# Performance work log

Measured on AMD Instinct MI355X. Metric: run time of the kernel, lower is better.

Reference implementation:

```python
import jax, jax.numpy as jnp
import numpy as np

B, T, H, DEPTH = 16, 2048, 256, 3

def setup_inputs() -> dict:
    key = jax.random.key(0)
    ks = jax.random.split(key, 5)
    x = jax.random.normal(ks[0], (B, T, H), dtype=jnp.float32)
    seq_lens = jax.random.randint(ks[1], (B,), 1, T + 1, dtype=jnp.int32)
    s = 1.0 / np.sqrt(H)
    W_ih = jax.random.uniform(ks[2], (DEPTH, H, H), jnp.float32, -s, s)
    W_hh = jax.random.uniform(ks[3], (DEPTH, H, H), jnp.float32, -s, s)
    b = jax.random.uniform(ks[4], (DEPTH, H), jnp.float32, -s, s)
    return {"x": x, "seq_lens": seq_lens, "W_ih": W_ih, "W_hh": W_hh, "b": b}

def reference(x, seq_lens, W_ih, W_hh, b):
    # x: [B, T, D], stacked depth-3 single-state recurrent cells:
    #   h[t,k] = tanh(inp @ W_ih[k]^T + h[t-1,k] @ W_hh[k]^T + b[k])
    # where inp = x[t] for k==0 else h[t,k-1]; h[-1,k] = 0 (init_state).
    Bx, Tx, D = x.shape
    depth = W_ih.shape[0]
    h0 = jnp.zeros((depth, Bx, D), dtype=x.dtype)

    def step(h_prev, x_t):  # h_prev: [depth, B, H], x_t: [B, D]
        inp = x_t
        hs = []
        for k in range(depth):
            hk = jnp.tanh(inp @ W_ih[k].T + h_prev[k] @ W_hh[k].T + b[k])
            hs.append(hk)
            inp = hk
        h_new = jnp.stack(hs)  # [depth, B, H]
        return h_new, h_new

    _, ys = jax.lax.scan(step, h0, jnp.swapaxes(x, 0, 1))  # ys: [T, depth, B, H]
    out = jnp.transpose(ys, (2, 0, 1, 3))  # [B, T, depth, H]
    # positions past each sequence's length are never written (stay zero)
    mask = (jnp.arange(Tx)[None, :] < seq_lens[:, None])[:, :, None, None]
    return out * mask.astype(out.dtype)
```

## Files before the change

kernel.cpp:

```cpp
#include <hip/hip_runtime.h>
#include <stdint.h>


#define TT 2048
#define HH 256

typedef _Float16 h16x8 __attribute__((ext_vector_type(8)));
typedef float f32x4 __attribute__((ext_vector_type(4)));

__device__ __forceinline__ unsigned pkrtz(float a, float b) {
  return __builtin_bit_cast(unsigned, __builtin_amdgcn_cvt_pkrtz(a, b));
}

__device__ __forceinline__ float tanh_fast(float x) {
  float xm = fmaxf(x, -15.0f);
  float e = __builtin_amdgcn_exp2f(xm * -2.88539008177793f);
  float r = __builtin_amdgcn_rcpf(1.0f + e);
  return __builtin_fmaf(-2.0f * e, r, 1.0f);
}

__device__ __forceinline__ void spin_ge(int* p, int need) {
  while (__hip_atomic_load(p, __ATOMIC_ACQUIRE, __HIP_MEMORY_SCOPE_AGENT) < need)
    __builtin_amdgcn_s_sleep(2);
}

__device__ __forceinline__ void light_barrier() {
  asm volatile("s_waitcnt expcnt(0) lgkmcnt(0)" ::: "memory");
  __builtin_amdgcn_s_barrier();
}

__global__ __launch_bounds__(512, 2)
void stacked_rnn(const float* __restrict__ x,
                 const int* __restrict__ seq_lens,
                 const float* __restrict__ Wih,
                 const float* __restrict__ Whh,
                 const float* __restrict__ bias,
                 float* __restrict__ out,
                 int* flags) {
  const int ks = blockIdx.x;
  const int tid = (int)threadIdx.x;
  const int w = tid >> 6;
  const int lane = tid & 63;
  const int q = lane >> 4;
  const int n = lane & 15;

  __shared__ __align__(16) unsigned short Bsm[2][8192];

  int* flag_up = flags + (ks - 1) * 64;
  int* flag_me = flags + ks * 64;

  h16x8 wf[2][16];
  {
    const float* wih_s = Wih + ks * (HH * HH);
    const float* whh_s = Whh + ks * (HH * HH);
#pragma unroll
    for (int mti = 0; mti < 2; ++mti) {
      const int fA = w * 32 + mti * 16 + n;
#pragma unroll
      for (int kt = 0; kt < 16; ++kt) {
        const int col = (kt & 7) * 32 + q * 8;
        const float* src = (kt < 8) ? (wih_s + fA * HH + col)
                                    : (whh_s + fA * HH + col);
        float4 a0 = ((const float4*)src)[0];
        float4 a1 = ((const float4*)src)[1];
        h16x8 f;
        f[0] = (_Float16)a0.x; f[1] = (_Float16)a0.y;
        f[2] = (_Float16)a0.z; f[3] = (_Float16)a0.w;
        f[4] = (_Float16)a1.x; f[5] = (_Float16)a1.y;
        f[6] = (_Float16)a1.z; f[7] = (_Float16)a1.w;
        wf[mti][kt] = f;
      }
    }
  }

  f32x4 biasv[2];
#pragma unroll
  for (int mti = 0; mti < 2; ++mti)
#pragma unroll
    for (int r = 0; r < 4; ++r)
      biasv[mti][r] = bias[ks * HH + w * 32 + mti * 16 + q * 4 + r];

  const int sl = seq_lens[n];

  const int rdE = (q * 16 + (n ^ q)) * 8;
  const int rdO = (q * 16 + (n ^ q ^ 4)) * 8;

  int hofs[2];
#pragma unroll
  for (int mti = 0; mti < 2; ++mti) {
    const int u = (8 + w) * 4 + mti * 2 + (q >> 1);
    hofs[mti] = (u * 16 + (n ^ (u & 7))) * 8 + (q & 1) * 4;
  }

  const int n_l = tid >> 5;
  const int k8  = tid & 31;
  const int u_l = (k8 >> 2) * 4 + (k8 & 3);
  const int ldst = (u_l * 16 + (n_l ^ (u_l & 7))) * 8;

  const float* src_base;
  int src_stride;
  if (ks == 0) {
    src_base = x + ((n_l * TT) << 8) + (k8 << 3);
    src_stride = HH;
  } else {
    src_base = out + (((n_l * TT) * 3 + (ks - 1)) << 8) + (k8 << 3);
    src_stride = 3 * HH;
  }

  ((uint4*)&Bsm[0][4096])[tid] = make_uint4(0, 0, 0, 0);
  if (ks > 0 && tid == 0) spin_ge(flag_up, 18);
  __syncthreads();

  {
    float4 c0 = ((const float4*)src_base)[0];
    float4 c1 = ((const float4*)src_base)[1];
    *(uint4*)&Bsm[0][ldst] = make_uint4(pkrtz(c0.x, c0.y), pkrtz(c0.z, c0.w),
                                        pkrtz(c1.x, c1.y), pkrtz(c1.z, c1.w));
  }
  float4 pfB0 = ((const float4*)(src_base + src_stride))[0];
  float4 pfB1 = ((const float4*)(src_base + src_stride))[1];
  const float* src_pf = src_base + 2 * src_stride;
  __syncthreads();

  float* outp = out + ((n * TT) * 3 + ks) * HH + w * 32 + q * 4;

  for (int t = 0; t < TT; ++t) {
    unsigned short* Bp = Bsm[t & 1];
    unsigned short* Bq = Bsm[(t & 1) ^ 1];

    if ((t & 7) == 0 && t > 0 && ks < 2 && tid == 0)
      __hip_atomic_store(flag_me, t, __ATOMIC_RELEASE,
                         __HIP_MEMORY_SCOPE_AGENT);
    if ((t & 15) == 0 && t > 0 && ks > 0) {
      if (tid == 0) {
        int need = t + 18;
        if (need > TT) need = TT;
        spin_ge(flag_up, need);
      }
      __syncthreads();
    }

    float4 pfA0, pfA1;
    const bool more2 = (t + 2 < TT);
    if (more2) {
      pfA0 = ((const float4*)src_pf)[0];
      pfA1 = ((const float4*)src_pf)[1];
    }
    src_pf += src_stride;

    f32x4 acc[2] = {biasv[0], biasv[1]};
#pragma unroll
    for (int kt = 0; kt < 16; ++kt) {
      const int ofs = ((kt & 1) ? rdO : rdE) + kt * 512;
      h16x8 bf = *(const h16x8*)&Bp[ofs];
      acc[0] = __builtin_amdgcn_mfma_f32_16x16x32_f16(wf[0][kt], bf, acc[0], 0, 0, 0);
      acc[1] = __builtin_amdgcn_mfma_f32_16x16x32_f16(wf[1][kt], bf, acc[1], 0, 0, 0);
    }

    const bool live = (t < sl);
    uint2 hpk[2];
#pragma unroll
    for (int mti = 0; mti < 2; ++mti) {
      float h0 = tanh_fast(acc[mti][0]);
      float h1 = tanh_fast(acc[mti][1]);
      float h2 = tanh_fast(acc[mti][2]);
      float h3 = tanh_fast(acc[mti][3]);
      hpk[mti].x = pkrtz(h0, h1);
      hpk[mti].y = pkrtz(h2, h3);
      float4 od;
      od.x = live ? h0 : 0.0f;
      od.y = live ? h1 : 0.0f;
      od.z = live ? h2 : 0.0f;
      od.w = live ? h3 : 0.0f;
      *(float4*)(outp + mti * 16) = od;
    }
    outp += 3 * HH;

    if (t + 1 < TT) {
      *(uint4*)&Bq[ldst] = make_uint4(pkrtz(pfB0.x, pfB0.y), pkrtz(pfB0.z, pfB0.w),
                                      pkrtz(pfB1.x, pfB1.y), pkrtz(pfB1.z, pfB1.w));
      *(uint2*)&Bq[hofs[0]] = hpk[0];
      *(uint2*)&Bq[hofs[1]] = hpk[1];
      if (more2) { pfB0 = pfA0; pfB1 = pfA1; }
    }

    if ((t & 7) == 7) {
      __syncthreads();
    } else {
      light_barrier();
    }
  }

  if (ks < 2 && tid == 0)
    __hip_atomic_store(flag_me, TT, __ATOMIC_RELEASE, __HIP_MEMORY_SCOPE_AGENT);
}

extern "C" void kernel_launch(void* const* d_in, const int* in_sizes, int n_in,
                              void* d_out, int out_size, void* d_ws, size_t ws_size,
                              hipStream_t stream) {
  (void)in_sizes; (void)n_in; (void)out_size; (void)ws_size;
  const float* x   = (const float*)d_in[0];
  const int*   sl  = (const int*)d_in[1];
  const float* wih = (const float*)d_in[2];
  const float* whh = (const float*)d_in[3];
  const float* b   = (const float*)d_in[4];

  (void)hipMemsetAsync(d_ws, 0, 1024, stream);
  hipLaunchKernelGGL(stacked_rnn, dim3(3), dim3(512), 0, stream,
                     x, sl, wih, whh, b, (float*)d_out, (int*)d_ws);
}
```

Measured before the change: 2.242 ms.

## Split waves into input-projection producers and recurrent-math consumers with LDS handoff

New measurement: 7.356 ms. +228.2%, slower.

```diff
diff --git a/kernel.cpp b/kernel.cpp
--- a/kernel.cpp
+++ b/kernel.cpp
@@ -10,6 +10,12 @@
 
 __device__ __forceinline__ unsigned pkrtz(float a, float b) {
   return __builtin_bit_cast(unsigned, __builtin_amdgcn_cvt_pkrtz(a, b));
+}
+
+__device__ __forceinline__ h16x8 pack8(float4 a, float4 b) {
+  uint4 u = make_uint4(pkrtz(a.x, a.y), pkrtz(a.z, a.w),
+                       pkrtz(b.x, b.y), pkrtz(b.z, b.w));
+  return __builtin_bit_cast(h16x8, u);
 }
 
 __device__ __forceinline__ float tanh_fast(float x) {
@@ -39,28 +45,28 @@
                  int* flags) {
   const int ks = blockIdx.x;
   const int tid = (int)threadIdx.x;
-  const int w = tid >> 6;
+  const int w8 = tid >> 6;
+  const bool is_math = (w8 < 4);
+  const int mw = w8 & 3;
   const int lane = tid & 63;
   const int q = lane >> 4;
   const int n = lane & 15;
 
-  __shared__ __align__(16) unsigned short Bsm[2][8192];
+  __shared__ __align__(16) unsigned short Hsm[2][4096];
+  __shared__ __align__(16) float Psm[2][4096];
 
   int* flag_up = flags + (ks - 1) * 64;
   int* flag_me = flags + ks * 64;
 
-  h16x8 wf[2][16];
+  h16x8 wf[4][8];
   {
-    const float* wih_s = Wih + ks * (HH * HH);
-    const float* whh_s = Whh + ks * (HH * HH);
-#pragma unroll
-    for (int mti = 0; mti < 2; ++mti) {
-      const int fA = w * 32 + mti * 16 + n;
-#pragma unroll
-      for (int kt = 0; kt < 16; ++kt) {
-        const int col = (kt & 7) * 32 + q * 8;
-        const float* src = (kt < 8) ? (wih_s + fA * HH + col)
-                                    : (whh_s + fA * HH + col);
+    const float* wsrc = (is_math ? Whh : Wih) + ks * (HH * HH);
+#pragma unroll
+    for (int mti = 0; mti < 4; ++mti) {
+      const int fA = mw * 64 + mti * 16 + n;
+#pragma unroll
+      for (int kt = 0; kt < 8; ++kt) {
+        const float* src = wsrc + fA * HH + kt * 32 + q * 8;
         float4 a0 = ((const float4*)src)[0];
         float4 a1 = ((const float4*)src)[1];
         h16x8 f;
@@ -73,61 +79,61 @@
     }
   }
 
-  f32x4 biasv[2];
-#pragma unroll
-  for (int mti = 0; mti < 2; ++mti)
+  f32x4 biasv[4];
+#pragma unroll
+  for (int mti = 0; mti < 4; ++mti)
 #pragma unroll
     for (int r = 0; r < 4; ++r)
-      biasv[mti][r] = bias[ks * HH + w * 32 + mti * 16 + q * 4 + r];
+      biasv[mti][r] = bias[ks * HH + mw * 64 + mti * 16 + q * 4 + r];
 
   const int sl = seq_lens[n];
 
   const int rdE = (q * 16 + (n ^ q)) * 8;
   const int rdO = (q * 16 + (n ^ q ^ 4)) * 8;
-
-  int hofs[2];
-#pragma unroll
-  for (int mti = 0; mti < 2; ++mti) {
-    const int u = (8 + w) * 4 + mti * 2 + (q >> 1);
+  int hofs[4];
+#pragma unroll
+  for (int mti = 0; mti < 4; ++mti) {
+    const int u = mw * 8 + mti * 2 + (q >> 1);
     hofs[mti] = (u * 16 + (n ^ (u & 7))) * 8 + (q & 1) * 4;
   }
-
-  const int n_l = tid >> 5;
-  const int k8  = tid & 31;
-  const int u_l = (k8 >> 2) * 4 + (k8 & 3);
-  const int ldst = (u_l * 16 + (n_l ^ (u_l & 7))) * 8;
-
-  const float* src_base;
-  int src_stride;
-  if (ks == 0) {
-    src_base = x + ((n_l * TT) << 8) + (k8 << 3);
-    src_stride = HH;
-  } else {
-    src_base = out + (((n_l * TT) * 3 + (ks - 1)) << 8) + (k8 << 3);
-    src_stride = 3 * HH;
-  }
-
-  ((uint4*)&Bsm[0][4096])[tid] = make_uint4(0, 0, 0, 0);
+  const int pofs = mw * 256 + lane * 4;
+
+  const float* ibase;
+  int istr;
+  if (ks == 0) { ibase = x + n * (TT * HH) + q * 8; istr = HH; }
+  else { ibase = out + (n * (TT * 3) + (ks - 1)) * HH + q * 8; istr = 3 * HH; }
+
+  ((uint4*)&Hsm[0][0])[tid] = make_uint4(0, 0, 0, 0);
   if (ks > 0 && tid == 0) spin_ge(flag_up, 18);
   __syncthreads();
 
-  {
-    float4 c0 = ((const float4*)src_base)[0];
-    float4 c1 = ((const float4*)src_base)[1];
-    *(uint4*)&Bsm[0][ldst] = make_uint4(pkrtz(c0.x, c0.y), pkrtz(c0.z, c0.w),
-                                        pkrtz(c1.x, c1.y), pkrtz(c1.z, c1.w));
-  }
-  float4 pfB0 = ((const float4*)(src_base + src_stride))[0];
-  float4 pfB1 = ((const float4*)(src_base + src_stride))[1];
-  const float* src_pf = src_base + 2 * src_stride;
+  h16x8 bfr[8];
+  if (!is_math) {
+    f32x4 a0 = biasv[0], a1 = biasv[1], a2 = biasv[2], a3 = biasv[3];
+#pragma unroll
+    for (int kt = 0; kt < 8; ++kt) {
+      const float* sp = ibase + kt * 32;
+      h16x8 bf = pack8(((const float4*)sp)[0], ((const float4*)(sp + 4))[0]);
+      a0 = __builtin_amdgcn_mfma_f32_16x16x32_f16(wf[0][kt], bf, a0, 0, 0, 0);
+      a1 = __builtin_amdgcn_mfma_f32_16x16x32_f16(wf[1][kt], bf, a1, 0, 0, 0);
+      a2 = __builtin_amdgcn_mfma_f32_16x16x32_f16(wf[2][kt], bf, a2, 0, 0, 0);
+      a3 = __builtin_amdgcn_mfma_f32_16x16x32_f16(wf[3][kt], bf, a3, 0, 0, 0);
+    }
+    *(f32x4*)&Psm[0][0 * 1024 + pofs] = a0;
+    *(f32x4*)&Psm[0][1 * 1024 + pofs] = a1;
+    *(f32x4*)&Psm[0][2 * 1024 + pofs] = a2;
+    *(f32x4*)&Psm[0][3 * 1024 + pofs] = a3;
+#pragma unroll
+    for (int kt = 0; kt < 8; ++kt) {
+      const float* sp = ibase + istr + kt * 32;
+      bfr[kt] = pack8(((const float4*)sp)[0], ((const float4*)(sp + 4))[0]);
+    }
+  }
   __syncthreads();
 
-  float* outp = out + ((n * TT) * 3 + ks) * HH + w * 32 + q * 4;
+  float* outp = out + (n * (TT * 3) + ks) * HH + mw * 64 + q * 4;
 
   for (int t = 0; t < TT; ++t) {
-    unsigned short* Bp = Bsm[t & 1];
-    unsigned short* Bq = Bsm[(t & 1) ^ 1];
-
     if ((t & 7) == 0 && t > 0 && ks < 2 && tid == 0)
       __hip_atomic_store(flag_me, t, __ATOMIC_RELEASE,
                          __HIP_MEMORY_SCOPE_AGENT);
@@ -140,48 +146,89 @@
       __syncthreads();
     }
 
-    float4 pfA0, pfA1;
-    const bool more2 = (t + 2 < TT);
-    if (more2) {
-      pfA0 = ((const float4*)src_pf)[0];
-      pfA1 = ((const float4*)src_pf)[1];
-    }
-    src_pf += src_stride;
-
-    f32x4 acc[2] = {biasv[0], biasv[1]};
-#pragma unroll
-    for (int kt = 0; kt < 16; ++kt) {
-      const int ofs = ((kt & 1) ? rdO : rdE) + kt * 512;
-      h16x8 bf = *(const h16x8*)&Bp[ofs];
-      acc[0] = __builtin_amdgcn_mfma_f32_16x16x32_f16(wf[0][kt], bf, acc[0], 0, 0, 0);
-      acc[1] = __builtin_amdgcn_mfma_f32_16x16x32_f16(wf[1][kt], bf, acc[1], 0, 0, 0);
-    }
-
-    const bool live = (t < sl);
-    uint2 hpk[2];
-#pragma unroll
-    for (int mti = 0; mti < 2; ++mti) {
-      float h0 = tanh_fast(acc[mti][0]);
-      float h1 = tanh_fast(acc[mti][1]);
-      float h2 = tanh_fast(acc[mti][2]);
-      float h3 = tanh_fast(acc[mti][3]);
-      hpk[mti].x = pkrtz(h0, h1);
-      hpk[mti].y = pkrtz(h2, h3);
-      float4 od;
-      od.x = live ? h0 : 0.0f;
-      od.y = live ? h1 : 0.0f;
-      od.z = live ? h2 : 0.0f;
-      od.w = live ? h3 : 0.0f;
-      *(float4*)(outp + mti * 16) = od;
-    }
-    outp += 3 * HH;
-
-    if (t + 1 < TT) {
-      *(uint4*)&Bq[ldst] = make_uint4(pkrtz(pfB0.x, pfB0.y), pkrtz(pfB0.z, pfB0.w),
-                                      pkrtz(pfB1.x, pfB1.y), pkrtz(pfB1.z, pfB1.w));
-      *(uint2*)&Bq[hofs[0]] = hpk[0];
-      *(uint2*)&Bq[hofs[1]] = hpk[1];
-      if (more2) { pfB0 = pfA0; pfB1 = pfA1; }
+    if (is_math) {
+      const float* Pp = &Psm[t & 1][0];
+      f32x4 ac0 = *(const f32x4*)&Pp[0 * 1024 + pofs];
+      f32x4 ac1 = *(const f32x4*)&Pp[1 * 1024 + pofs];
+      f32x4 ac2 = *(const f32x4*)&Pp[2 * 1024 + pofs];
+      f32x4 ac3 = *(const f32x4*)&Pp[3 * 1024 + pofs];
+      const unsigned short* Hp = Hsm[t & 1];
+#pragma unroll
+      for (int kt = 0; kt < 8; ++kt) {
+        const int ofs = ((kt & 1) ? rdO : rdE) + kt * 512;
+        h16x8 hf = *(const h16x8*)&Hp[ofs];
+        ac0 = __builtin_amdgcn_mfma_f32_16x16x32_f16(wf[0][kt], hf, ac0, 0, 0, 0);
+        ac1 = __builtin_amdgcn_mfma_f32_16x16x32_f16(wf[1][kt], hf, ac1, 0, 0, 0);
+        ac2 = __builtin_amdgcn_mfma_f32_16x16x32_f16(wf[2][kt], hf, ac2, 0, 0, 0);
+        ac3 = __builtin_amdgcn_mfma_f32_16x16x32_f16(wf[3][kt], hf, ac3, 0, 0, 0);
+      }
+      const bool live = (t < sl);
+      const bool wr = (t + 1 < TT);
+      unsigned short* Hq = Hsm[(t & 1) ^ 1];
+      f32x4 acc[4] = {ac0, ac1, ac2, ac3};
+#pragma unroll
+      for (int mti = 0; mti < 4; ++mti) {
+        float h0 = tanh_fast(acc[mti][0]);
+        float h1 = tanh_fast(acc[mti][1]);
+        float h2 = tanh_fast(acc[mti][2]);
+        float h3 = tanh_fast(acc[mti][3]);
+        uint2 pk;
+        pk.x = pkrtz(h0, h1);
+        pk.y = pkrtz(h2, h3);
+        float4 od;
+        od.x = live ? h0 : 0.0f;
+        od.y = live ? h1 : 0.0f;
+        od.z = live ? h2 : 0.0f;
+        od.w = live ? h3 : 0.0f;
+        *(float4*)(outp + mti * 16) = od;
+        if (wr) *(uint2*)&Hq[hofs[mti]] = pk;
+      }
+      outp += 3 * HH;
+    } else {
+      const bool more1 = (t + 1 < TT);
+      const bool more2 = (t + 2 < TT);
+      const float* s = ibase + (t + 2) * istr;
+      float4 ra0, rb0, ra1, rb1, ra2, rb2, ra3, rb3;
+      if (more2) {
+        ra0 = ((const float4*)(s + 0 * 32))[0]; rb0 = ((const float4*)(s + 0 * 32 + 4))[0];
+        ra1 = ((const float4*)(s + 1 * 32))[0]; rb1 = ((const float4*)(s + 1 * 32 + 4))[0];
+        ra2 = ((const float4*)(s + 2 * 32))[0]; rb2 = ((const float4*)(s + 2 * 32 + 4))[0];
+        ra3 = ((const float4*)(s + 3 * 32))[0]; rb3 = ((const float4*)(s + 3 * 32 + 4))[0];
+      }
+      if (more1) {
+        f32x4 a0 = biasv[0], a1 = biasv[1], a2 = biasv[2], a3 = biasv[3];
+#pragma unroll
+        for (int kt = 0; kt < 4; ++kt) {
+          a0 = __builtin_amdgcn_mfma_f32_16x16x32_f16(wf[0][kt], bfr[kt], a0, 0, 0, 0);
+          a1 = __builtin_amdgcn_mfma_f32_16x16x32_f16(wf[1][kt], bfr[kt], a1, 0, 0, 0);
+          a2 = __builtin_amdgcn_mfma_f32_16x16x32_f16(wf[2][kt], bfr[kt], a2, 0, 0, 0);
+          a3 = __builtin_amdgcn_mfma_f32_16x16x32_f16(wf[3][kt], bfr[kt], a3, 0, 0, 0);
+        }
+        if (more2) {
+          bfr[0] = pack8(ra0, rb0); bfr[1] = pack8(ra1, rb1);
+          bfr[2] = pack8(ra2, rb2); bfr[3] = pack8(ra3, rb3);
+          ra0 = ((const float4*)(s + 4 * 32))[0]; rb0 = ((const float4*)(s + 4 * 32 + 4))[0];
+          ra1 = ((const float4*)(s + 5 * 32))[0]; rb1 = ((const float4*)(s + 5 * 32 + 4))[0];
+          ra2 = ((const float4*)(s + 6 * 32))[0]; rb2 = ((const float4*)(s + 6 * 32 + 4))[0];
+          ra3 = ((const float4*)(s + 7 * 32))[0]; rb3 = ((const float4*)(s + 7 * 32 + 4))[0];
+        }
+#pragma unroll
+        for (int kt = 4; kt < 8; ++kt) {
+          a0 = __builtin_amdgcn_mfma_f32_16x16x32_f16(wf[0][kt], bfr[kt], a0, 0, 0, 0);
+          a1 = __builtin_amdgcn_mfma_f32_16x16x32_f16(wf[1][kt], bfr[kt], a1, 0, 0, 0);
+          a2 = __builtin_amdgcn_mfma_f32_16x16x32_f16(wf[2][kt], bfr[kt], a2, 0, 0, 0);
+          a3 = __builtin_amdgcn_mfma_f32_16x16x32_f16(wf[3][kt], bfr[kt], a3, 0, 0, 0);
+        }
+        float* Pq = &Psm[(t & 1) ^ 1][0];
+        *(f32x4*)&Pq[0 * 1024 + pofs] = a0;
+        *(f32x4*)&Pq[1 * 1024 + pofs] = a1;
+        *(f32x4*)&Pq[2 * 1024 + pofs] = a2;
+        *(f32x4*)&Pq[3 * 1024 + pofs] = a3;
+        if (more2) {
+          bfr[4] = pack8(ra0, rb0); bfr[5] = pack8(ra1, rb1);
+          bfr[6] = pack8(ra2, rb2); bfr[7] = pack8(ra3, rb3);
+        }
+      }
     }
 
     if ((t & 7) == 7) {
```

## Stream fp16 input images from a producer block into MFMA-ready register fragments

Applied to the files above, without the earlier changes.

After: 2.914 ms. +30.0%, slower.

```diff
diff --git a/kernel.cpp b/kernel.cpp
--- a/kernel.cpp
+++ b/kernel.cpp
@@ -10,6 +10,11 @@
 
 __device__ __forceinline__ unsigned pkrtz(float a, float b) {
   return __builtin_bit_cast(unsigned, __builtin_amdgcn_cvt_pkrtz(a, b));
+}
+
+__device__ __forceinline__ uint4 pack8u(float4 a, float4 b) {
+  return make_uint4(pkrtz(a.x, a.y), pkrtz(a.z, a.w),
+                    pkrtz(b.x, b.y), pkrtz(b.z, b.w));
 }
 
 __device__ __forceinline__ float tanh_fast(float x) {
@@ -30,24 +35,51 @@
 }
 
 __global__ __launch_bounds__(512, 2)
-void stacked_rnn(const float* __restrict__ x,
-                 const int* __restrict__ seq_lens,
-                 const float* __restrict__ Wih,
-                 const float* __restrict__ Whh,
-                 const float* __restrict__ bias,
-                 float* __restrict__ out,
-                 int* flags) {
-  const int ks = blockIdx.x;
+void stacked_rnn_img(const float* __restrict__ x,
+                     const int* __restrict__ seq_lens,
+                     const float* __restrict__ Wih,
+                     const float* __restrict__ Whh,
+                     const float* __restrict__ bias,
+                     float* __restrict__ out,
+                     int* flags) {
+  const int bid = (int)blockIdx.x;
   const int tid = (int)threadIdx.x;
+  char* const img_all = (char*)flags + 4096;
+
+  if (bid == 3) {
+    const int n_l = tid >> 5;
+    const int k8  = tid & 31;
+    const float* sx = x + n_l * (TT * HH) + (k8 << 3);
+    char* dst = img_all + ((k8 >> 2) * 1024 + (((k8 & 3) * 16) + n_l) * 16);
+    int* fMe = flags + 3 * 64;
+    for (int c = 0; c < TT; c += 16) {
+#pragma unroll 4
+      for (int tt = 0; tt < 16; ++tt) {
+        const float* sp = sx + (c + tt) * HH;
+        float4 a = ((const float4*)sp)[0];
+        float4 b = ((const float4*)sp)[1];
+        *(uint4*)(dst + (size_t)(c + tt) * 8192) = pack8u(a, b);
+      }
+      __syncthreads();
+      if (tid == 0)
+        __hip_atomic_store(fMe, c + 16, __ATOMIC_RELEASE,
+                           __HIP_MEMORY_SCOPE_AGENT);
+    }
+    return;
+  }
+
+  const int ks = bid;
   const int w = tid >> 6;
   const int lane = tid & 63;
   const int q = lane >> 4;
   const int n = lane & 15;
 
-  __shared__ __align__(16) unsigned short Bsm[2][8192];
-
-  int* flag_up = flags + (ks - 1) * 64;
+  __shared__ __align__(16) unsigned short Hsm[2][4096];
+
   int* flag_me = flags + ks * 64;
+  int* flag_up = flags + ((ks == 0) ? 3 : (ks - 1)) * 64;
+  const char* img_rd = img_all + (size_t)ks * TT * 8192;
+  char* img_wr = img_all + (size_t)((ks < 2) ? (ks + 1) : 2) * TT * 8192;
 
   h16x8 wf[2][16];
   {
@@ -84,80 +116,66 @@
 
   const int rdE = (q * 16 + (n ^ q)) * 8;
   const int rdO = (q * 16 + (n ^ q ^ 4)) * 8;
-
-  int hofs[2];
+  int hofs[2], mofs[2];
 #pragma unroll
   for (int mti = 0; mti < 2; ++mti) {
-    const int u = (8 + w) * 4 + mti * 2 + (q >> 1);
+    const int u = w * 4 + mti * 2 + (q >> 1);
     hofs[mti] = (u * 16 + (n ^ (u & 7))) * 8 + (q & 1) * 4;
-  }
-
-  const int n_l = tid >> 5;
-  const int k8  = tid & 31;
-  const int u_l = (k8 >> 2) * 4 + (k8 & 3);
-  const int ldst = (u_l * 16 + (n_l ^ (u_l & 7))) * 8;
-
-  const float* src_base;
-  int src_stride;
-  if (ks == 0) {
-    src_base = x + ((n_l * TT) << 8) + (k8 << 3);
-    src_stride = HH;
-  } else {
-    src_base = out + (((n_l * TT) * 3 + (ks - 1)) << 8) + (k8 << 3);
-    src_stride = 3 * HH;
-  }
-
-  ((uint4*)&Bsm[0][4096])[tid] = make_uint4(0, 0, 0, 0);
-  if (ks > 0 && tid == 0) spin_ge(flag_up, 18);
+    mofs[mti] = w * 1024 + ((mti * 2 + (q >> 1)) * 16 + n) * 16 + (q & 1) * 8;
+  }
+
+  ((uint4*)&Hsm[0][0])[tid] = make_uint4(0, 0, 0, 0);
+  if (tid == 0) spin_ge(flag_up, 17);
   __syncthreads();
 
-  {
-    float4 c0 = ((const float4*)src_base)[0];
-    float4 c1 = ((const float4*)src_base)[1];
-    *(uint4*)&Bsm[0][ldst] = make_uint4(pkrtz(c0.x, c0.y), pkrtz(c0.z, c0.w),
-                                        pkrtz(c1.x, c1.y), pkrtz(c1.z, c1.w));
-  }
-  float4 pfB0 = ((const float4*)(src_base + src_stride))[0];
-  float4 pfB1 = ((const float4*)(src_base + src_stride))[1];
-  const float* src_pf = src_base + 2 * src_stride;
-  __syncthreads();
-
-  float* outp = out + ((n * TT) * 3 + ks) * HH + w * 32 + q * 4;
+  uint4 ifr[8];
+#pragma unroll
+  for (int j = 0; j < 8; ++j)
+    ifr[j] = *(const uint4*)(img_rd + j * 1024 + (lane << 4));
+  const char* ird = img_rd + 8192;
+
+  float* outp = out + (n * (TT * 3) + ks) * HH + w * 32 + q * 4;
+  char* mwp = img_wr;
 
   for (int t = 0; t < TT; ++t) {
-    unsigned short* Bp = Bsm[t & 1];
-    unsigned short* Bq = Bsm[(t & 1) ^ 1];
+    const unsigned short* Hp = Hsm[t & 1];
+    unsigned short* Hq = Hsm[(t & 1) ^ 1];
 
     if ((t & 7) == 0 && t > 0 && ks < 2 && tid == 0)
       __hip_atomic_store(flag_me, t, __ATOMIC_RELEASE,
                          __HIP_MEMORY_SCOPE_AGENT);
-    if ((t & 15) == 0 && t > 0 && ks > 0) {
+    if ((t & 15) == 0 && t > 0) {
       if (tid == 0) {
-        int need = t + 18;
+        int need = t + 17;
         if (need > TT) need = TT;
         spin_ge(flag_up, need);
       }
       __syncthreads();
     }
 
-    float4 pfA0, pfA1;
-    const bool more2 = (t + 2 < TT);
-    if (more2) {
-      pfA0 = ((const float4*)src_pf)[0];
-      pfA1 = ((const float4*)src_pf)[1];
-    }
-    src_pf += src_stride;
-
     f32x4 acc[2] = {biasv[0], biasv[1]};
 #pragma unroll
-    for (int kt = 0; kt < 16; ++kt) {
-      const int ofs = ((kt & 1) ? rdO : rdE) + kt * 512;
-      h16x8 bf = *(const h16x8*)&Bp[ofs];
+    for (int kt = 0; kt < 8; ++kt) {
+      h16x8 bf = __builtin_bit_cast(h16x8, ifr[kt]);
       acc[0] = __builtin_amdgcn_mfma_f32_16x16x32_f16(wf[0][kt], bf, acc[0], 0, 0, 0);
       acc[1] = __builtin_amdgcn_mfma_f32_16x16x32_f16(wf[1][kt], bf, acc[1], 0, 0, 0);
     }
+#pragma unroll
+    for (int kt = 0; kt < 8; ++kt) {
+      h16x8 hf = *(const h16x8*)&Hp[((kt & 1) ? rdO : rdE) + kt * 512];
+      acc[0] = __builtin_amdgcn_mfma_f32_16x16x32_f16(wf[0][8 + kt], hf, acc[0], 0, 0, 0);
+      acc[1] = __builtin_amdgcn_mfma_f32_16x16x32_f16(wf[1][8 + kt], hf, acc[1], 0, 0, 0);
+    }
+
+    if (t + 1 < TT) {
+#pragma unroll
+      for (int j = 0; j < 8; ++j)
+        ifr[j] = *(const uint4*)(ird + j * 1024 + (lane << 4));
+    }
+    ird += 8192;
 
     const bool live = (t < sl);
+    const bool wr = (t + 1 < TT);
     uint2 hpk[2];
 #pragma unroll
     for (int mti = 0; mti < 2; ++mti) {
@@ -173,12 +191,169 @@
       od.z = live ? h2 : 0.0f;
       od.w = live ? h3 : 0.0f;
       *(float4*)(outp + mti * 16) = od;
+      if (ks < 2) *(uint2*)(mwp + mofs[mti]) = hpk[mti];
+      if (wr) *(uint2*)&Hq[hofs[mti]] = hpk[mti];
     }
     outp += 3 * HH;
+    mwp += 8192;
+
+    if ((t & 7) == 7) {
+      __syncthreads();
+    } else {
+      light_barrier();
+    }
+  }
+
+  if (ks < 2 && tid == 0)
+    __hip_atomic_store(flag_me, TT, __ATOMIC_RELEASE, __HIP_MEMORY_SCOPE_AGENT);
+}
+
+__global__ __launch_bounds__(512, 2)
+void stacked_rnn_v3(const float* __restrict__ x,
+                    const int* __restrict__ seq_lens,
+                    const float* __restrict__ Wih,
+                    const float* __restrict__ Whh,
+                    const float* __restrict__ bias,
+                    float* __restrict__ out,
+                    int* flags) {
+  const int ks = blockIdx.x;
+  const int tid = (int)threadIdx.x;
+  const int w = tid >> 6;
+  const int lane = tid & 63;
+  const int q = lane >> 4;
+  const int n = lane & 15;
+
+  __shared__ __align__(16) unsigned short Bsm[2][8192];
+
+  int* flag_up = flags + (ks - 1) * 64;
+  int* flag_me = flags + ks * 64;
+
+  h16x8 wf[2][16];
+  {
+    const float* wih_s = Wih + ks * (HH * HH);
+    const float* whh_s = Whh + ks * (HH * HH);
+#pragma unroll
+    for (int mti = 0; mti < 2; ++mti) {
+      const int fA = w * 32 + mti * 16 + n;
+#pragma unroll
+      for (int kt = 0; kt < 16; ++kt) {
+        const int col = (kt & 7) * 32 + q * 8;
+        const float* src = (kt < 8) ? (wih_s + fA * HH + col)
+                                    : (whh_s + fA * HH + col);
+        float4 a0 = ((const float4*)src)[0];
+        float4 a1 = ((const float4*)src)[1];
+        h16x8 f;
+        f[0] = (_Float16)a0.x; f[1] = (_Float16)a0.y;
+        f[2] = (_Float16)a0.z; f[3] = (_Float16)a0.w;
+        f[4] = (_Float16)a1.x; f[5] = (_Float16)a1.y;
+        f[6] = (_Float16)a1.z; f[7] = (_Float16)a1.w;
+        wf[mti][kt] = f;
+      }
+    }
+  }
+
+  f32x4 biasv[2];
+#pragma unroll
+  for (int mti = 0; mti < 2; ++mti)
+#pragma unroll
+    for (int r = 0; r < 4; ++r)
+      biasv[mti][r] = bias[ks * HH + w * 32 + mti * 16 + q * 4 + r];
+
+  const int sl = seq_lens[n];
+  const int rdE = (q * 16 + (n ^ q)) * 8;
+  const int rdO = (q * 16 + (n ^ q ^ 4)) * 8;
+  int hofs[2];
+#pragma unroll
+  for (int mti = 0; mti < 2; ++mti) {
+    const int u = (8 + w) * 4 + mti * 2 + (q >> 1);
+    hofs[mti] = (u * 16 + (n ^ (u & 7))) * 8 + (q & 1) * 4;
+  }
+
+  const int n_l = tid >> 5;
+  const int k8  = tid & 31;
+  const int u_l = (k8 >> 2) * 4 + (k8 & 3);
+  const int ldst = (u_l * 16 + (n_l ^ (u_l & 7))) * 8;
+
+  const float* src_base;
+  int src_stride;
+  if (ks == 0) {
+    src_base = x + ((n_l * TT) << 8) + (k8 << 3);
+    src_stride = HH;
+  } else {
+    src_base = out + (((n_l * TT) * 3 + (ks - 1)) << 8) + (k8 << 3);
+    src_stride = 3 * HH;
+  }
+
+  ((uint4*)&Bsm[0][4096])[tid] = make_uint4(0, 0, 0, 0);
+  if (ks > 0 && tid == 0) spin_ge(flag_up, 18);
+  __syncthreads();
+
+  {
+    float4 c0 = ((const float4*)src_base)[0];
+    float4 c1 = ((const float4*)src_base)[1];
+    *(uint4*)&Bsm[0][ldst] = pack8u(c0, c1);
+  }
+  float4 pfB0 = ((const float4*)(src_base + src_stride))[0];
+  float4 pfB1 = ((const float4*)(src_base + src_stride))[1];
+  const float* src_pf = src_base + 2 * src_stride;
+  __syncthreads();
+
+  float* outp = out + ((n * TT) * 3 + ks) * HH + w * 32 + q * 4;
+
+  for (int t = 0; t < TT; ++t) {
+    unsigned short* Bp = Bsm[t & 1];
+    unsigned short* Bq = Bsm[(t & 1) ^ 1];
+
+    if ((t & 7) == 0 && t > 0 && ks < 2 && tid == 0)
+      __hip_atomic_store(flag_me, t, __ATOMIC_RELEASE,
+                         __HIP_MEMORY_SCOPE_AGENT);
+    if ((t & 15) == 0 && t > 0 && ks > 0) {
+      if (tid == 0) {
+        int need = t + 18;
+        if (need > TT) need = TT;
+        spin_ge(flag_up, need);
+      }
+      __syncthreads();
+    }
+
+    float4 pfA0, pfA1;
+    const bool more2 = (t + 2 < TT);
+    if (more2) {
+      pfA0 = ((const float4*)src_pf)[0];
+      pfA1 = ((const float4*)src_pf)[1];
+    }
+    src_pf += src_stride;
+
+    f32x4 acc[2] = {biasv[0], biasv[1]};
+#pragma unroll
+    for (int kt = 0; kt < 16; ++kt) {
+      const int ofs = ((kt & 1) ? rdO : rdE) + kt * 512;
+      h16x8 bf = *(const h16x8*)&Bp[ofs];
+      acc[0] = __builtin_amdgcn_mfma_f32_16x16x32_f16(wf[0][kt], bf, acc[0], 0, 0, 0);
+      acc[1] = __builtin_amdgcn_mfma_f32_16x16x32_f16(wf[1][kt], bf, acc[1], 0, 0, 0);
+    }
+
+    const bool live = (t < sl);
+    uint2 hpk[2];
+#pragma unroll
+    for (int mti = 0; mti < 2; ++mti) {
+      float h0 = tanh_fast(acc[mti][0]);
+      float h1 = tanh_fast(acc[mti][1]);
+      float h2 = tanh_fast(acc[mti][2]);
+      float h3 = tanh_fast(acc[mti][3]);
+      hpk[mti].x = pkrtz(h0, h1);
+      hpk[mti].y = pkrtz(h2, h3);
+      float4 od;
+      od.x = live ? h0 : 0.0f;
+      od.y = live ? h1 : 0.0f;
+      od.z = live ? h2 : 0.0f;
+      od.w = live ? h3 : 0.0f;
+      *(float4*)(outp + mti * 16) = od;
+    }
+    outp += 3 * HH;
 
     if (t + 1 < TT) {
-      *(uint4*)&Bq[ldst] = make_uint4(pkrtz(pfB0.x, pfB0.y), pkrtz(pfB0.z, pfB0.w),
-                                      pkrtz(pfB1.x, pfB1.y), pkrtz(pfB1.z, pfB1.w));
+      *(uint4*)&Bq[ldst] = pack8u(pfB0, pfB1);
       *(uint2*)&Bq[hofs[0]] = hpk[0];
       *(uint2*)&Bq[hofs[1]] = hpk[1];
       if (more2) { pfB0 = pfA0; pfB1 = pfA1; }
@@ -198,14 +373,20 @@
 extern "C" void kernel_launch(void* const* d_in, const int* in_sizes, int n_in,
                               void* d_out, int out_size, void* d_ws, size_t ws_size,
                               hipStream_t stream) {
-  (void)in_sizes; (void)n_in; (void)out_size; (void)ws_size;
+  (void)in_sizes; (void)n_in; (void)out_size;
   const float* x   = (const float*)d_in[0];
   const int*   sl  = (const int*)d_in[1];
   const float* wih = (const float*)d_in[2];
   const float* whh = (const float*)d_in[3];
   const float* b   = (const float*)d_in[4];
 
-  (void)hipMemsetAsync(d_ws, 0, 1024, stream);
-  hipLaunchKernelGGL(stacked_rnn, dim3(3), dim3(512), 0, stream,
-                     x, sl, wih, whh, b, (float*)d_out, (int*)d_ws);
-}
+  (void)hipMemsetAsync(d_ws, 0, 4096, stream);
+  const size_t need = 4096 + (size_t)3 * TT * 8192;
+  if (ws_size >= need) {
+    hipLaunchKernelGGL(stacked_rnn_img, dim3(4), dim3(512), 0, stream,
+                       x, sl, wih, whh, b, (float*)d_out, (int*)d_ws);
+  } else {
+    hipLaunchKernelGGL(stacked_rnn_v3, dim3(3), dim3(512), 0, stream,
+                       x, sl, wih, whh, b, (float*)d_out, (int*)d_ws);
+  }
+}
```

## Split input and hidden LDS buffers and precompute next-step input projection

Applied to the files above, without the earlier changes.

Result: slower. 2.414 ms (+7.7%).

```diff
diff --git a/kernel.cpp b/kernel.cpp
--- a/kernel.cpp
+++ b/kernel.cpp
@@ -10,6 +10,11 @@
 
 __device__ __forceinline__ unsigned pkrtz(float a, float b) {
   return __builtin_bit_cast(unsigned, __builtin_amdgcn_cvt_pkrtz(a, b));
+}
+
+__device__ __forceinline__ uint4 pack8u(float4 a, float4 b) {
+  return make_uint4(pkrtz(a.x, a.y), pkrtz(a.z, a.w),
+                    pkrtz(b.x, b.y), pkrtz(b.z, b.w));
 }
 
 __device__ __forceinline__ float tanh_fast(float x) {
@@ -44,7 +49,8 @@
   const int q = lane >> 4;
   const int n = lane & 15;
 
-  __shared__ __align__(16) unsigned short Bsm[2][8192];
+  __shared__ __align__(16) unsigned short Hsm[2][4096];
+  __shared__ __align__(16) unsigned short Ism[2][4096];
 
   int* flag_up = flags + (ks - 1) * 64;
   int* flag_me = flags + ks * 64;
@@ -88,14 +94,13 @@
   int hofs[2];
 #pragma unroll
   for (int mti = 0; mti < 2; ++mti) {
-    const int u = (8 + w) * 4 + mti * 2 + (q >> 1);
+    const int u = w * 4 + mti * 2 + (q >> 1);
     hofs[mti] = (u * 16 + (n ^ (u & 7))) * 8 + (q & 1) * 4;
   }
 
   const int n_l = tid >> 5;
   const int k8  = tid & 31;
-  const int u_l = (k8 >> 2) * 4 + (k8 & 3);
-  const int ldst = (u_l * 16 + (n_l ^ (u_l & 7))) * 8;
+  const int ldstI = (k8 * 16 + (n_l ^ (k8 & 7))) * 8;
 
   const float* src_base;
   int src_stride;
@@ -107,33 +112,41 @@
     src_stride = 3 * HH;
   }
 
-  ((uint4*)&Bsm[0][4096])[tid] = make_uint4(0, 0, 0, 0);
-  if (ks > 0 && tid == 0) spin_ge(flag_up, 18);
+  ((uint4*)&Hsm[0][0])[tid] = make_uint4(0, 0, 0, 0);
+  if (ks > 0 && tid == 0) spin_ge(flag_up, 19);
   __syncthreads();
 
   {
     float4 c0 = ((const float4*)src_base)[0];
     float4 c1 = ((const float4*)src_base)[1];
-    *(uint4*)&Bsm[0][ldst] = make_uint4(pkrtz(c0.x, c0.y), pkrtz(c0.z, c0.w),
-                                        pkrtz(c1.x, c1.y), pkrtz(c1.z, c1.w));
-  }
-  float4 pfB0 = ((const float4*)(src_base + src_stride))[0];
-  float4 pfB1 = ((const float4*)(src_base + src_stride))[1];
-  const float* src_pf = src_base + 2 * src_stride;
+    *(uint4*)&Ism[0][ldstI] = pack8u(c0, c1);
+    float4 d0 = ((const float4*)(src_base + src_stride))[0];
+    float4 d1 = ((const float4*)(src_base + src_stride))[1];
+    *(uint4*)&Ism[1][ldstI] = pack8u(d0, d1);
+  }
+  float4 pfB0 = ((const float4*)(src_base + 2 * src_stride))[0];
+  float4 pfB1 = ((const float4*)(src_base + 2 * src_stride))[1];
+  const float* src_pf = src_base + 3 * src_stride;
   __syncthreads();
 
-  float* outp = out + ((n * TT) * 3 + ks) * HH + w * 32 + q * 4;
+  f32x4 accC0 = biasv[0], accC1 = biasv[1];
+#pragma unroll
+  for (int kt = 0; kt < 8; ++kt) {
+    h16x8 bf = *(const h16x8*)&Ism[0][((kt & 1) ? rdO : rdE) + kt * 512];
+    accC0 = __builtin_amdgcn_mfma_f32_16x16x32_f16(wf[0][kt], bf, accC0, 0, 0, 0);
+    accC1 = __builtin_amdgcn_mfma_f32_16x16x32_f16(wf[1][kt], bf, accC1, 0, 0, 0);
+  }
+  __syncthreads();
+
+  float* outp = out + (n * (TT * 3) + ks) * HH + w * 32 + q * 4;
 
   for (int t = 0; t < TT; ++t) {
-    unsigned short* Bp = Bsm[t & 1];
-    unsigned short* Bq = Bsm[(t & 1) ^ 1];
-
     if ((t & 7) == 0 && t > 0 && ks < 2 && tid == 0)
       __hip_atomic_store(flag_me, t, __ATOMIC_RELEASE,
                          __HIP_MEMORY_SCOPE_AGENT);
     if ((t & 15) == 0 && t > 0 && ks > 0) {
       if (tid == 0) {
-        int need = t + 18;
+        int need = t + 19;
         if (need > TT) need = TT;
         spin_ge(flag_up, need);
       }
@@ -141,24 +154,33 @@
     }
 
     float4 pfA0, pfA1;
-    const bool more2 = (t + 2 < TT);
-    if (more2) {
+    const bool more3 = (t + 3 < TT);
+    if (more3) {
       pfA0 = ((const float4*)src_pf)[0];
       pfA1 = ((const float4*)src_pf)[1];
     }
     src_pf += src_stride;
 
-    f32x4 acc[2] = {biasv[0], biasv[1]};
-#pragma unroll
-    for (int kt = 0; kt < 16; ++kt) {
-      const int ofs = ((kt & 1) ? rdO : rdE) + kt * 512;
-      h16x8 bf = *(const h16x8*)&Bp[ofs];
-      acc[0] = __builtin_amdgcn_mfma_f32_16x16x32_f16(wf[0][kt], bf, acc[0], 0, 0, 0);
-      acc[1] = __builtin_amdgcn_mfma_f32_16x16x32_f16(wf[1][kt], bf, acc[1], 0, 0, 0);
+    const unsigned short* Hp = Hsm[t & 1];
+#pragma unroll
+    for (int kt = 0; kt < 8; ++kt) {
+      h16x8 hf = *(const h16x8*)&Hp[((kt & 1) ? rdO : rdE) + kt * 512];
+      accC0 = __builtin_amdgcn_mfma_f32_16x16x32_f16(wf[0][8 + kt], hf, accC0, 0, 0, 0);
+      accC1 = __builtin_amdgcn_mfma_f32_16x16x32_f16(wf[1][8 + kt], hf, accC1, 0, 0, 0);
+    }
+
+    const bool more1 = (t + 1 < TT);
+    h16x8 ifr[8];
+    if (more1) {
+      const unsigned short* Ip = Ism[(t + 1) & 1];
+#pragma unroll
+      for (int kt = 0; kt < 8; ++kt)
+        ifr[kt] = *(const h16x8*)&Ip[((kt & 1) ? rdO : rdE) + kt * 512];
     }
 
     const bool live = (t < sl);
     uint2 hpk[2];
+    f32x4 acc[2] = {accC0, accC1};
 #pragma unroll
     for (int mti = 0; mti < 2; ++mti) {
       float h0 = tanh_fast(acc[mti][0]);
@@ -176,13 +198,24 @@
     }
     outp += 3 * HH;
 
-    if (t + 1 < TT) {
-      *(uint4*)&Bq[ldst] = make_uint4(pkrtz(pfB0.x, pfB0.y), pkrtz(pfB0.z, pfB0.w),
-                                      pkrtz(pfB1.x, pfB1.y), pkrtz(pfB1.z, pfB1.w));
-      *(uint2*)&Bq[hofs[0]] = hpk[0];
-      *(uint2*)&Bq[hofs[1]] = hpk[1];
-      if (more2) { pfB0 = pfA0; pfB1 = pfA1; }
-    }
+    if (more1) {
+      f32x4 aN0 = biasv[0], aN1 = biasv[1];
+#pragma unroll
+      for (int kt = 0; kt < 8; ++kt) {
+        aN0 = __builtin_amdgcn_mfma_f32_16x16x32_f16(wf[0][kt], ifr[kt], aN0, 0, 0, 0);
+        aN1 = __builtin_amdgcn_mfma_f32_16x16x32_f16(wf[1][kt], ifr[kt], aN1, 0, 0, 0);
+      }
+      accC0 = aN0; accC1 = aN1;
+    }
+
+    if (more1) {
+      unsigned short* Hq = Hsm[(t & 1) ^ 1];
+      *(uint2*)&Hq[hofs[0]] = hpk[0];
+      *(uint2*)&Hq[hofs[1]] = hpk[1];
+    }
+    if (t + 2 < TT)
+      *(uint4*)&Ism[t & 1][ldstI] = pack8u(pfB0, pfB1);
+    if (more3) { pfB0 = pfA0; pfB1 = pfA1; }
 
     if ((t & 7) == 7) {
       __syncthreads();
```
